# Performance work log

Measured on AMD Instinct MI355X. Metric: run time of the kernel, lower is better.

The kernel has to match this reference:

```python
import jax, jax.numpy as jnp
import numpy as np

DIM = 1024
NUM_HEADS = 16
HEAD_DIM = DIM // NUM_HEADS
SCALE = HEAD_DIM ** -0.5


def setup_inputs() -> dict:
    key = jax.random.key(0)
    ks = jax.random.split(key, 5)
    B, N, C = 2, 2048, DIM
    x = jax.random.normal(ks[0], (B, N, C), dtype=jnp.float32)
    s = 1.0 / np.sqrt(C)
    W_qkv = jax.random.normal(ks[1], (C, 3 * C), dtype=jnp.float32) * s
    b_qkv = jax.random.normal(ks[2], (3 * C,), dtype=jnp.float32) * 0.01
    W_proj = jax.random.normal(ks[3], (C, C), dtype=jnp.float32) * s
    b_proj = jax.random.normal(ks[4], (C,), dtype=jnp.float32) * 0.01
    return {"x": x, "W_qkv": W_qkv, "b_qkv": b_qkv, "W_proj": W_proj, "b_proj": b_proj}


def reference(x, W_qkv, b_qkv, W_proj, b_proj):
    B, N, C = x.shape
    qkv = x @ W_qkv + b_qkv                      # [B, N, 3C]
    qkv = qkv.reshape(B, N, 3, NUM_HEADS, HEAD_DIM)
    qkv = jnp.transpose(qkv, (2, 0, 3, 1, 4))    # [3, B, H, N, hd]
    # Faithful to source quirk: q = k = v = qkv[2]
    v = qkv[2]
    q = v
    k = v
    attn = jnp.einsum('bhnd,bhmd->bhnm', q, k) * SCALE
    attn = jax.nn.softmax(attn, axis=-1)
    out = jnp.einsum('bhnm,bhmd->bhnd', attn, v)  # [B, H, N, hd]
    out = jnp.transpose(out, (0, 2, 1, 3)).reshape(B, N, C)
    return out @ W_proj + b_proj
```

## Files before the change

### kernel.cpp

```cpp
#include <hip/hip_runtime.h>

typedef __bf16    bf16x4 __attribute__((ext_vector_type(4)));
typedef __bf16    bf16x8 __attribute__((ext_vector_type(8)));
typedef _Float16  f16x2  __attribute__((ext_vector_type(2)));
typedef _Float16  f16x4  __attribute__((ext_vector_type(4)));
typedef _Float16  f16x8  __attribute__((ext_vector_type(8)));
typedef float     f32x4  __attribute__((ext_vector_type(4)));

#define MFMA16x16x32 __builtin_amdgcn_mfma_f32_16x16x32_bf16
#define MFMA16x16x16F __builtin_amdgcn_mfma_f32_16x16x16f16

__device__ __forceinline__ void gload_lds16(const void* g, void* l) {
  __builtin_amdgcn_global_load_lds((const __attribute__((address_space(1))) void*)g,
                                   (__attribute__((address_space(3))) void*)l, 16, 0, 0);
}

__device__ __forceinline__ f16x2 pkrtz(float a, float b) {
  return __builtin_bit_cast(f16x2, __builtin_amdgcn_cvt_pkrtz(a, b));
}

__global__ __launch_bounds__(256) void prep_all(const float* __restrict__ x,
                                                const float* __restrict__ Wqkv,
                                                const float* __restrict__ Wproj,
                                                __bf16* __restrict__ xb,
                                                __bf16* __restrict__ WvT,
                                                __bf16* __restrict__ WpT) {
  __shared__ float tile[64][65];
  const int t = threadIdx.x;
  if (blockIdx.z == 2) {
    const int bid = blockIdx.x * 16 + blockIdx.y;
#pragma unroll
    for (int c = 0; c < 16; c++) {
      int gid = (bid * 16 + c) * 256 + t;
      float4 v = ((const float4*)x)[gid];
      bf16x4 o;
      o.x = (__bf16)v.x; o.y = (__bf16)v.y; o.z = (__bf16)v.z; o.w = (__bf16)v.w;
      *(bf16x4*)&xb[(size_t)gid * 4] = o;
    }
    return;
  }
  const float* src; __bf16* dst; int ld, c0;
  if (blockIdx.z == 0) { src = Wqkv; dst = WvT; ld = 3072; c0 = 2048; }
  else                 { src = Wproj; dst = WpT; ld = 1024; c0 = 0; }
  const int k0 = blockIdx.x * 64, n0 = blockIdx.y * 64;
#pragma unroll
  for (int i = 0; i < 4; i++) {
    int idx = t + i * 256; int r = idx >> 4, g = idx & 15;
    float4 v = *(const float4*)&src[(size_t)(k0 + r) * ld + c0 + n0 + g * 4];
    tile[r][g * 4 + 0] = v.x; tile[r][g * 4 + 1] = v.y;
    tile[r][g * 4 + 2] = v.z; tile[r][g * 4 + 3] = v.w;
  }
  __syncthreads();
#pragma unroll
  for (int i = 0; i < 4; i++) {
    int idx = t + i * 256; int n = idx >> 4, g = idx & 15;
    bf16x4 o;
    o.x = (__bf16)tile[g * 4 + 0][n]; o.y = (__bf16)tile[g * 4 + 1][n];
    o.z = (__bf16)tile[g * 4 + 2][n]; o.w = (__bf16)tile[g * 4 + 3][n];
    *(bf16x4*)&dst[(size_t)(n0 + n) * 1024 + k0 + g * 4] = o;
  }
}

#define STAGE_TILE(bi, kk)                                            \
  { char* buf_ = (char*)lds + (bi) * 24576;                           \
    const __bf16* a_ = pA + (kk) * 64;                                \
    const __bf16* b_ = pB + (kk) * 64;                                \
    gload_lds16(a_,          buf_ + t * 16);                          \
    gload_lds16(a_ + 32 * K, buf_ + 4096  + t * 16);                  \
    gload_lds16(a_ + 64 * K, buf_ + 8192  + t * 16);                  \
    gload_lds16(a_ + 96 * K, buf_ + 12288 + t * 16);                  \
    gload_lds16(b_,          buf_ + 16384 + t * 16);                  \
    gload_lds16(b_ + 32 * K, buf_ + 20480 + t * 16); }

__global__ __launch_bounds__(256, 2) void gemm_v(const __bf16* __restrict__ xb,
                                                 const __bf16* __restrict__ WvT,
                                                 const float* __restrict__ bias,
                                                 __bf16* __restrict__ V,
                                                 _Float16* __restrict__ Vt) {
  constexpr int K = 1024;
  __shared__ char lds[3 * 24576];
  const int t = threadIdx.x, w = t >> 6, l = t & 63, lr = l & 15, quad = l >> 4;
  const int wr = w >> 1, wc = w & 1;
  const int wgid = blockIdx.x;
  const int xcd = wgid & 7, sub = wgid >> 3;
  const int mb = xcd * 4 + (sub & 3), nb = sub >> 2;
  const int m0 = mb * 128, n0 = nb * 64;

  const int row0 = t >> 3;
  const int scol = (t & 7) ^ (row0 & 7);
  const __bf16* pA = xb  + (size_t)(m0 + row0) * K + scol * 8;
  const __bf16* pB = WvT + (size_t)(n0 + row0) * K + scol * 8;

  f32x4 acc[4][2] = {};
  int aoff[4][2], boff[2][2];
#pragma unroll
  for (int mi = 0; mi < 4; mi++)
#pragma unroll
    for (int ks = 0; ks < 2; ks++)
      aoff[mi][ks] = (wr * 64 + mi * 16 + lr) * 128 + (((ks * 4 + quad) ^ (lr & 7)) * 16);
#pragma unroll
  for (int nc = 0; nc < 2; nc++)
#pragma unroll
    for (int ks = 0; ks < 2; ks++)
      boff[nc][ks] = 16384 + (wc * 32 + nc * 16 + lr) * 128 + (((ks * 4 + quad) ^ (lr & 7)) * 16);

  STAGE_TILE(0, 0);
  STAGE_TILE(1, 1);
  for (int it = 0; it < 16; ++it) {
    if (it < 15) { asm volatile("s_waitcnt vmcnt(6)" ::: "memory"); }
    else         { asm volatile("s_waitcnt vmcnt(0)" ::: "memory"); }
    __builtin_amdgcn_sched_barrier(0);
    __builtin_amdgcn_s_barrier();
    if (it + 2 < 16) STAGE_TILE((it + 2) % 3, it + 2);
    const char* buf = (const char*)lds + (it % 3) * 24576;
    bf16x8 af[4][2], bv[2][2];
#pragma unroll
    for (int mi = 0; mi < 4; mi++)
#pragma unroll
      for (int ks = 0; ks < 2; ks++)
        af[mi][ks] = *(const bf16x8*)(buf + aoff[mi][ks]);
#pragma unroll
    for (int nc = 0; nc < 2; nc++)
#pragma unroll
      for (int ks = 0; ks < 2; ks++)
        bv[nc][ks] = *(const bf16x8*)(buf + boff[nc][ks]);
#pragma unroll
    for (int mi = 0; mi < 4; mi++)
#pragma unroll
      for (int nc = 0; nc < 2; nc++)
#pragma unroll
        for (int ks = 0; ks < 2; ks++)
          acc[mi][nc] = MFMA16x16x32(af[mi][ks], bv[nc][ks], acc[mi][nc], 0, 0, 0);
  }
#pragma unroll
  for (int mi = 0; mi < 4; mi++) {
    const int grow0 = m0 + wr * 64 + mi * 16 + quad * 4;
    const int b_ = grow0 >> 11, tok0 = grow0 & 2047;
#pragma unroll
    for (int nc = 0; nc < 2; nc++) {
      const int d = wc * 32 + nc * 16 + lr;
      const int gcol = n0 + d;
      float bb = bias[gcol];
      float v0 = acc[mi][nc][0] + bb, v1 = acc[mi][nc][1] + bb;
      float v2 = acc[mi][nc][2] + bb, v3 = acc[mi][nc][3] + bb;
      V[(size_t)(grow0 + 0) * 1024 + gcol] = (__bf16)v0;
      V[(size_t)(grow0 + 1) * 1024 + gcol] = (__bf16)v1;
      V[(size_t)(grow0 + 2) * 1024 + gcol] = (__bf16)v2;
      V[(size_t)(grow0 + 3) * 1024 + gcol] = (__bf16)v3;
      f16x2 lo = pkrtz(v0, v1), hi = pkrtz(v2, v3);
      f16x4 pv; pv[0] = lo[0]; pv[1] = lo[1]; pv[2] = hi[0]; pv[3] = hi[1];
      *(f16x4*)&Vt[((size_t)(b_ * 16 + nb) * 64 + d) * 2048 + tok0] = pv;
    }
  }
}

__global__ __launch_bounds__(256, 2) void gemm_proj(const __bf16* __restrict__ A,
                                                    const __bf16* __restrict__ Bt,
                                                    const float* __restrict__ bias,
                                                    float* __restrict__ outp) {
  constexpr int K = 1024, Nn = 1024;
  __shared__ char lds[3 * 24576];
  const int t = threadIdx.x, w = t >> 6, l = t & 63, lr = l & 15, quad = l >> 4;
  const int wr = w >> 1, wc = w & 1;
  const int wgid = blockIdx.x;
  const int xcd = wgid & 7, sub = wgid >> 3;
  const int mb = xcd * 4 + (sub & 3), nb = sub >> 2;
  const int m0 = mb * 128, n0 = nb * 64;

  const int row0 = t >> 3;
  const int scol = (t & 7) ^ (row0 & 7);
  const __bf16* pA = A  + (size_t)(m0 + row0) * K + scol * 8;
  const __bf16* pB = Bt + (size_t)(n0 + row0) * K + scol * 8;

  f32x4 acc[4][2] = {};
  int aoff[4][2], boff[2][2];
#pragma unroll
  for (int mi = 0; mi < 4; mi++)
#pragma unroll
    for (int ks = 0; ks < 2; ks++)
      aoff[mi][ks] = (wr * 64 + mi * 16 + lr) * 128 + (((ks * 4 + quad) ^ (lr & 7)) * 16);
#pragma unroll
  for (int nc = 0; nc < 2; nc++)
#pragma unroll
    for (int ks = 0; ks < 2; ks++)
      boff[nc][ks] = 16384 + (wc * 32 + nc * 16 + lr) * 128 + (((ks * 4 + quad) ^ (lr & 7)) * 16);

  STAGE_TILE(0, 0);
  STAGE_TILE(1, 1);
  for (int it = 0; it < 16; ++it) {
    if (it < 15) { asm volatile("s_waitcnt vmcnt(6)" ::: "memory"); }
    else         { asm volatile("s_waitcnt vmcnt(0)" ::: "memory"); }
    __builtin_amdgcn_sched_barrier(0);
    __builtin_amdgcn_s_barrier();
    if (it + 2 < 16) STAGE_TILE((it + 2) % 3, it + 2);
    const char* buf = (const char*)lds + (it % 3) * 24576;
    bf16x8 af[4][2], bv[2][2];
#pragma unroll
    for (int mi = 0; mi < 4; mi++)
#pragma unroll
      for (int ks = 0; ks < 2; ks++)
        af[mi][ks] = *(const bf16x8*)(buf + aoff[mi][ks]);
#pragma unroll
    for (int nc = 0; nc < 2; nc++)
#pragma unroll
      for (int ks = 0; ks < 2; ks++)
        bv[nc][ks] = *(const bf16x8*)(buf + boff[nc][ks]);
#pragma unroll
    for (int mi = 0; mi < 4; mi++)
#pragma unroll
      for (int nc = 0; nc < 2; nc++)
#pragma unroll
        for (int ks = 0; ks < 2; ks++)
          acc[mi][nc] = MFMA16x16x32(af[mi][ks], bv[nc][ks], acc[mi][nc], 0, 0, 0);
  }
#pragma unroll
  for (int mi = 0; mi < 4; mi++) {
    const int grow0 = m0 + wr * 64 + mi * 16 + quad * 4;
#pragma unroll
    for (int nc = 0; nc < 2; nc++) {
      const int gcol = n0 + wc * 32 + nc * 16 + lr;
      float bb = bias[gcol];
#pragma unroll
      for (int r = 0; r < 4; r++)
        outp[(size_t)(grow0 + r) * Nn + gcol] = acc[mi][nc][r] + bb;
    }
  }
}

__global__ __launch_bounds__(512, 4) void attn_kernel(const __bf16* __restrict__ V,
                                                      const _Float16* __restrict__ Vt,
                                                      __bf16* __restrict__ O) {
  __shared__ char lds[65536];
  const int t = threadIdx.x, w = t >> 6, l = t & 63, lr = l & 15, quad = l >> 4;
  const int bh = blockIdx.x, b = bh >> 4, h = bh & 15;
  const int qb = blockIdx.y * 128 + (w & 3) * 16;
  const int part = w >> 2;

  const __bf16* Vbh = V + (size_t)b * 2048 * 1024 + h * 64;
  const _Float16* Vtbh = Vt + (size_t)bh * 64 * 2048;

  bf16x8 qf[2][2];
#pragma unroll
  for (int sub = 0; sub < 2; sub++)
#pragma unroll
    for (int ks = 0; ks < 2; ks++)
      qf[sub][ks] = *(const bf16x8*)(Vbh + (size_t)(qb + sub * 64 + lr) * 1024 + ks * 32 + quad * 8);

  const int kva = t >> 3, ua = (t & 7) ^ (kva & 7);
  const __bf16* pK0 = Vbh + (size_t)kva * 1024 + ua * 8;
  const __bf16* pK1 = pK0 + (size_t)64 * 1024;
  const int kb_ = t >> 7, d_ = (t >> 1) & 63, qh = (t & 1) ^ ((d_ >> 2) & 1);
  const _Float16* pV0 = Vtbh + (size_t)d_ * 2048 + kb_ * 16 + qh * 8;
  const _Float16* pV1 = pV0 + 64;

  const int koff0 = lr * 128 + ((quad ^ (lr & 7)) * 16);
  const int koff1 = lr * 128 + (((4 + quad) ^ (lr & 7)) * 16);
  const int xq = (quad >> 1) ^ ((lr >> 2) & 1);
  const int voff = lr * 32 + xq * 16 + (quad & 1) * 8;

  f32x4 o[2][4] = {};
  f32x4 l5[2] = {};
  f16x4 ones; ones[0] = ones[1] = ones[2] = ones[3] = (_Float16)1.0f;
  const float Cc = 0.18033688011112042f;
  const float C8 = 11.541560327111707f;

  {
    char* base = lds;
    gload_lds16(pK0, base + t * 16);
    gload_lds16(pV0, base + 8192 + t * 16);
    gload_lds16(pK1, base + 16384 + t * 16);
    gload_lds16(pV1, base + 24576 + t * 16);
  }
  for (int it = 0; it < 16; ++it) {
    __syncthreads();
    if (it + 1 < 16) {
      pK0 += 131072; pK1 += 131072; pV0 += 128; pV1 += 128;
      char* base = lds + ((it + 1) & 1) * 32768;
      gload_lds16(pK0, base + t * 16);
      gload_lds16(pV0, base + 8192 + t * 16);
      gload_lds16(pK1, base + 16384 + t * 16);
      gload_lds16(pV1, base + 24576 + t * 16);
    }
    const char* Kb = lds + (it & 1) * 32768 + part * 16384;
    const char* Vb = Kb + 8192;

    f32x4 s[2][4] = {};
#pragma unroll
    for (int ks = 0; ks < 2; ks++) {
      const int ko = ks ? koff1 : koff0;
#pragma unroll
      for (int rb = 0; rb < 4; rb++) {
        bf16x8 kf = *(const bf16x8*)(Kb + ko + rb * 2048);
        s[0][rb] = MFMA16x16x32(kf, qf[0][ks], s[0][rb], 0, 0, 0);
        s[1][rb] = MFMA16x16x32(kf, qf[1][ks], s[1][rb], 0, 0, 0);
      }
    }

    f16x4 pf[2][4];
#pragma unroll
    for (int sub = 0; sub < 2; sub++)
#pragma unroll
      for (int rb = 0; rb < 4; rb++) {
        float p0 = __builtin_amdgcn_exp2f(s[sub][rb][0] * Cc - C8);
        float p1 = __builtin_amdgcn_exp2f(s[sub][rb][1] * Cc - C8);
        float p2 = __builtin_amdgcn_exp2f(s[sub][rb][2] * Cc - C8);
        float p3 = __builtin_amdgcn_exp2f(s[sub][rb][3] * Cc - C8);
        f16x2 lo = pkrtz(p0, p1);
        f16x2 hi = pkrtz(p2, p3);
        pf[sub][rb][0] = lo[0]; pf[sub][rb][1] = lo[1];
        pf[sub][rb][2] = hi[0]; pf[sub][rb][3] = hi[1];
      }

#pragma unroll
    for (int kb = 0; kb < 4; kb++) {
#pragma unroll
      for (int db = 0; db < 4; db++) {
        f16x4 vf = *(const f16x4*)(Vb + voff + db * 512 + kb * 2048);
        o[0][db] = MFMA16x16x16F(pf[0][kb], vf, o[0][db], 0, 0, 0);
        o[1][db] = MFMA16x16x16F(pf[1][kb], vf, o[1][db], 0, 0, 0);
      }
      l5[0] = MFMA16x16x16F(pf[0][kb], ones, l5[0], 0, 0, 0);
      l5[1] = MFMA16x16x16F(pf[1][kb], ones, l5[1], 0, 0, 0);
    }
  }

  __syncthreads();
  float* xch = (float*)lds;
  if (w >= 4) {
    float* dsto = xch + (w - 4) * 2048;
#pragma unroll
    for (int sub = 0; sub < 2; sub++)
#pragma unroll
      for (int db = 0; db < 4; db++)
        *(f32x4*)&dsto[(sub * 4 + db) * 256 + l * 4] = o[sub][db];
    float* dstl = xch + 8192 + (w - 4) * 512;
    *(f32x4*)&dstl[l * 4] = l5[0];
    *(f32x4*)&dstl[256 + l * 4] = l5[1];
  }
  __syncthreads();
  if (w < 4) {
    const float* srco = xch + w * 2048;
    const float* srcl = xch + 8192 + w * 512;
#pragma unroll
    for (int sub = 0; sub < 2; sub++) {
#pragma unroll
      for (int db = 0; db < 4; db++)
        o[sub][db] += *(const f32x4*)&srco[(sub * 4 + db) * 256 + l * 4];
      l5[sub] += *(const f32x4*)&srcl[sub * 256 + l * 4];
    }
#pragma unroll
    for (int sub = 0; sub < 2; sub++)
#pragma unroll
      for (int r = 0; r < 4; r++) {
        float lv = 1.0f / l5[sub][r];
        int token = b * 2048 + qb + sub * 64 + quad * 4 + r;
#pragma unroll
        for (int db = 0; db < 4; db++)
          O[(size_t)token * 1024 + h * 64 + db * 16 + lr] = (__bf16)(o[sub][db][r] * lv);
      }
  }
}

extern "C" void kernel_launch(void* const* d_in, const int* in_sizes, int n_in,
                              void* d_out, int out_size, void* d_ws, size_t ws_size,
                              hipStream_t stream) {
  (void)in_sizes; (void)n_in; (void)out_size; (void)ws_size;
  const float* x     = (const float*)d_in[0];
  const float* Wqkv  = (const float*)d_in[1];
  const float* bqkv  = (const float*)d_in[2];
  const float* Wproj = (const float*)d_in[3];
  const float* bproj = (const float*)d_in[4];

  char* ws = (char*)d_ws;
  __bf16*    V   = (__bf16*)(ws);
  _Float16*  Vt  = (_Float16*)(ws + (size_t)8  * 1048576);
  __bf16*    Ob  = (__bf16*)(ws + (size_t)16 * 1048576);
  __bf16*    xb  = (__bf16*)(ws + (size_t)16 * 1048576);
  __bf16*    WvT = (__bf16*)(ws + (size_t)24 * 1048576);
  __bf16*    WpT = (__bf16*)(ws + (size_t)26 * 1048576);

  prep_all<<<dim3(16, 16, 3), 256, 0, stream>>>(x, Wqkv, Wproj, xb, WvT, WpT);
  gemm_v<<<dim3(512), 256, 0, stream>>>(xb, WvT, bqkv + 2048, V, Vt);
  attn_kernel<<<dim3(32, 16), 512, 0, stream>>>(V, Vt, Ob);
  gemm_proj<<<dim3(512), 256, 0, stream>>>(Ob, WpT, bproj, (float*)d_out);
}
```

Measured before the change: 150.1 us.

## Repartition attention waves: 4 query subtiles per wave, 4-way KV split

Each wave now handles 64 query rows (4 subtiles) over a quarter of each KV tile instead of 32 rows over half. This raises reuse of each K/V fragment loaded from LDS across more MFMAs, cutting LDS reads per MFMA. The cost is twice the accumulator registers, which may hurt occupancy under launch_bounds(512,4), and a longer serialized 3-step cross-wave reduction with extra barriers at the end.

New measurement: 392.2 us. 2.61x slower.

```diff
diff --git a/kernel.cpp b/kernel.cpp
--- a/kernel.cpp
+++ b/kernel.cpp
@@ -233,18 +233,18 @@
   __shared__ char lds[65536];
   const int t = threadIdx.x, w = t >> 6, l = t & 63, lr = l & 15, quad = l >> 4;
   const int bh = blockIdx.x, b = bh >> 4, h = bh & 15;
-  const int qb = blockIdx.y * 128 + (w & 3) * 16;
-  const int part = w >> 2;
+  const int qw = w & 1, part = w >> 1;
+  const int qb = blockIdx.y * 128 + qw * 64;
 
   const __bf16* Vbh = V + (size_t)b * 2048 * 1024 + h * 64;
   const _Float16* Vtbh = Vt + (size_t)bh * 64 * 2048;
 
-  bf16x8 qf[2][2];
-#pragma unroll
-  for (int sub = 0; sub < 2; sub++)
-#pragma unroll
-    for (int ks = 0; ks < 2; ks++)
-      qf[sub][ks] = *(const bf16x8*)(Vbh + (size_t)(qb + sub * 64 + lr) * 1024 + ks * 32 + quad * 8);
+  bf16x8 qf[4][2];
+#pragma unroll
+  for (int sub = 0; sub < 4; sub++)
+#pragma unroll
+    for (int ks = 0; ks < 2; ks++)
+      qf[sub][ks] = *(const bf16x8*)(Vbh + (size_t)(qb + sub * 16 + lr) * 1024 + ks * 32 + quad * 8);
 
   const int kva = t >> 3, ua = (t & 7) ^ (kva & 7);
   const __bf16* pK0 = Vbh + (size_t)kva * 1024 + ua * 8;
@@ -257,9 +257,10 @@
   const int koff1 = lr * 128 + (((4 + quad) ^ (lr & 7)) * 16);
   const int xq = (quad >> 1) ^ ((lr >> 2) & 1);
   const int voff = lr * 32 + xq * 16 + (quad & 1) * 8;
-
-  f32x4 o[2][4] = {};
-  f32x4 l5[2] = {};
+  const int pbase = (part >> 1) * 16384 + (part & 1) * 4096;
+
+  f32x4 o[4][4] = {};
+  f32x4 l5[4] = {};
   f16x4 ones; ones[0] = ones[1] = ones[2] = ones[3] = (_Float16)1.0f;
   const float Cc = 0.18033688011112042f;
   const float C8 = 11.541560327111707f;
@@ -281,26 +282,27 @@
       gload_lds16(pK1, base + 16384 + t * 16);
       gload_lds16(pV1, base + 24576 + t * 16);
     }
-    const char* Kb = lds + (it & 1) * 32768 + part * 16384;
-    const char* Vb = Kb + 8192;
-
-    f32x4 s[2][4] = {};
+    const char* Kb = lds + (it & 1) * 32768 + pbase;
+    const char* Vb = lds + (it & 1) * 32768 + 8192 + pbase;
+
+    f32x4 s[4][2] = {};
 #pragma unroll
     for (int ks = 0; ks < 2; ks++) {
       const int ko = ks ? koff1 : koff0;
 #pragma unroll
-      for (int rb = 0; rb < 4; rb++) {
+      for (int rb = 0; rb < 2; rb++) {
         bf16x8 kf = *(const bf16x8*)(Kb + ko + rb * 2048);
-        s[0][rb] = MFMA16x16x32(kf, qf[0][ks], s[0][rb], 0, 0, 0);
-        s[1][rb] = MFMA16x16x32(kf, qf[1][ks], s[1][rb], 0, 0, 0);
-      }
-    }
-
-    f16x4 pf[2][4];
-#pragma unroll
-    for (int sub = 0; sub < 2; sub++)
-#pragma unroll
-      for (int rb = 0; rb < 4; rb++) {
+#pragma unroll
+        for (int sub = 0; sub < 4; sub++)
+          s[sub][rb] = MFMA16x16x32(kf, qf[sub][ks], s[sub][rb], 0, 0, 0);
+      }
+    }
+
+    f16x4 pf[4][2];
+#pragma unroll
+    for (int sub = 0; sub < 4; sub++)
+#pragma unroll
+      for (int rb = 0; rb < 2; rb++) {
         float p0 = __builtin_amdgcn_exp2f(s[sub][rb][0] * Cc - C8);
         float p1 = __builtin_amdgcn_exp2f(s[sub][rb][1] * Cc - C8);
         float p2 = __builtin_amdgcn_exp2f(s[sub][rb][2] * Cc - C8);
@@ -312,48 +314,56 @@
       }
 
 #pragma unroll
-    for (int kb = 0; kb < 4; kb++) {
+    for (int kb = 0; kb < 2; kb++) {
 #pragma unroll
       for (int db = 0; db < 4; db++) {
         f16x4 vf = *(const f16x4*)(Vb + voff + db * 512 + kb * 2048);
-        o[0][db] = MFMA16x16x16F(pf[0][kb], vf, o[0][db], 0, 0, 0);
-        o[1][db] = MFMA16x16x16F(pf[1][kb], vf, o[1][db], 0, 0, 0);
-      }
-      l5[0] = MFMA16x16x16F(pf[0][kb], ones, l5[0], 0, 0, 0);
-      l5[1] = MFMA16x16x16F(pf[1][kb], ones, l5[1], 0, 0, 0);
-    }
-  }
-
-  __syncthreads();
+#pragma unroll
+        for (int sub = 0; sub < 4; sub++)
+          o[sub][db] = MFMA16x16x16F(pf[sub][kb], vf, o[sub][db], 0, 0, 0);
+      }
+#pragma unroll
+      for (int sub = 0; sub < 4; sub++)
+        l5[sub] = MFMA16x16x16F(pf[sub][kb], ones, l5[sub], 0, 0, 0);
+    }
+  }
+
   float* xch = (float*)lds;
-  if (w >= 4) {
-    float* dsto = xch + (w - 4) * 2048;
-#pragma unroll
-    for (int sub = 0; sub < 2; sub++)
-#pragma unroll
-      for (int db = 0; db < 4; db++)
-        *(f32x4*)&dsto[(sub * 4 + db) * 256 + l * 4] = o[sub][db];
-    float* dstl = xch + 8192 + (w - 4) * 512;
-    *(f32x4*)&dstl[l * 4] = l5[0];
-    *(f32x4*)&dstl[256 + l * 4] = l5[1];
-  }
-  __syncthreads();
-  if (w < 4) {
-    const float* srco = xch + w * 2048;
-    const float* srcl = xch + 8192 + w * 512;
-#pragma unroll
-    for (int sub = 0; sub < 2; sub++) {
-#pragma unroll
-      for (int db = 0; db < 4; db++)
-        o[sub][db] += *(const f32x4*)&srco[(sub * 4 + db) * 256 + l * 4];
-      l5[sub] += *(const f32x4*)&srcl[sub * 256 + l * 4];
-    }
-#pragma unroll
-    for (int sub = 0; sub < 2; sub++)
+#pragma unroll
+  for (int p = 1; p < 4; p++) {
+    __syncthreads();
+    if (part == p) {
+      float* dsto = xch + qw * 4096;
+#pragma unroll
+      for (int sub = 0; sub < 4; sub++)
+#pragma unroll
+        for (int db = 0; db < 4; db++)
+          *(f32x4*)&dsto[(sub * 4 + db) * 256 + l * 4] = o[sub][db];
+      float* dstl = xch + 8192 + qw * 1024;
+#pragma unroll
+      for (int sub = 0; sub < 4; sub++)
+        *(f32x4*)&dstl[sub * 256 + l * 4] = l5[sub];
+    }
+    __syncthreads();
+    if (part == 0) {
+      const float* srco = xch + qw * 4096;
+      const float* srcl = xch + 8192 + qw * 1024;
+#pragma unroll
+      for (int sub = 0; sub < 4; sub++) {
+#pragma unroll
+        for (int db = 0; db < 4; db++)
+          o[sub][db] += *(const f32x4*)&srco[(sub * 4 + db) * 256 + l * 4];
+        l5[sub] += *(const f32x4*)&srcl[sub * 256 + l * 4];
+      }
+    }
+  }
+  if (part == 0) {
+#pragma unroll
+    for (int sub = 0; sub < 4; sub++)
 #pragma unroll
       for (int r = 0; r < 4; r++) {
         float lv = 1.0f / l5[sub][r];
-        int token = b * 2048 + qb + sub * 64 + quad * 4 + r;
+        int token = b * 2048 + qb + sub * 16 + quad * 4 + r;
 #pragma unroll
         for (int db = 0; db < 4; db++)
           O[(size_t)token * 1024 + h * 64 + db * 16 + lr] = (__bf16)(o[sub][db][r] * lv);
```
